# Performance work log

Measured on AMD Instinct MI355X. Metric: run time of the kernel, lower is better.

The kernel has to match this reference:

```python
import jax, jax.numpy as jnp
import numpy as np

N_NODES = 10000
W_DIM = 512
N_EDGES = 200000


def setup_inputs() -> dict:
    key = jax.random.key(0)
    k1, k2, k3 = jax.random.split(key, 3)
    z_drug = jax.random.normal(k1, (N_NODES, W_DIM), dtype=jnp.float32)
    # glorot-style init for the bilinear weight
    glorot_std = jnp.sqrt(2.0 / (W_DIM + W_DIM)).astype(jnp.float32)
    weight = jax.random.normal(k2, (W_DIM, W_DIM), dtype=jnp.float32) * glorot_std
    batch_edges = jax.random.randint(k3, (2, N_EDGES), 0, N_NODES, dtype=jnp.int64)
    return {"z_drug": z_drug, "weight": weight, "batch_edges": batch_edges}


def reference(z_drug, weight, batch_edges):
    # edge_type == 'drug_drug': both endpoints come from the drug table.
    row_embed = z_drug[batch_edges[0]]  # [E, d]
    col_embed = z_drug[batch_edges[1]]  # [E, d]
    # score_e = row_e @ W @ col_e  == diag((Z1 W) Z2^T) without the N x N blowup
    score = jnp.einsum('ed,df,ef->e', row_embed, weight, col_embed)
    return jax.nn.sigmoid(score)  # is_sigmoid=True default
```

## Files before the change

kernel.cpp:

```cpp
#include <hip/hip_runtime.h>
#include <math.h>

#define DIM     512
#define NNODES  10000
#define NEDGES  200000
#define MPAD    10048
#define NMB     157
#define NGRP    5
#define NB      (NGRP * NNODES)
#define SCAN_BLK 49
#define GEMM_GRID (NMB * 4)

using short8  = __attribute__((ext_vector_type(8))) short;
using floatx4 = __attribute__((ext_vector_type(4))) float;
using half8   = __attribute__((ext_vector_type(8))) _Float16;
using half2v  = __attribute__((ext_vector_type(2))) _Float16;

__device__ inline float dot2acc(half2v a, half2v b, float c) {
#if __has_builtin(__builtin_amdgcn_fdot2)
    return __builtin_amdgcn_fdot2(a, b, c, false);
#else
    return fmaf((float)a[0], (float)b[0], fmaf((float)a[1], (float)b[1], c));
#endif
}

#define PREP_ZBLK 2512
__global__ __launch_bounds__(256) void prep(const float* __restrict__ Z,
                                            const float* __restrict__ W,
                                            _Float16* __restrict__ Zh16,
                                            _Float16* __restrict__ Wh16t,
                                            int* __restrict__ counts) {
    const int b = blockIdx.x;
    const int t = threadIdx.x;

    if (b < 196) {
        int i = b * 256 + t;
        if (i < NB) counts[i] = 0;
    }

    if (b < PREP_ZBLK) {
        const int idx8 = (b * 256 + t) * 8;
        const int m = idx8 >> 9;
        float x[8];
        if (m < NNODES) {
            float4 v0 = *(const float4*)(Z + idx8);
            float4 v1 = *(const float4*)(Z + idx8 + 4);
            x[0]=v0.x; x[1]=v0.y; x[2]=v0.z; x[3]=v0.w;
            x[4]=v1.x; x[5]=v1.y; x[6]=v1.z; x[7]=v1.w;
        } else {
            #pragma unroll
            for (int j = 0; j < 8; ++j) x[j] = 0.f;
        }
        half8 h;
        #pragma unroll
        for (int j = 0; j < 8; ++j) h[j] = (_Float16)x[j];
        *(half8*)(Zh16 + idx8) = h;
    } else {
        __shared__ float tile[64][65];
        const int wb = b - PREP_ZBLK;
        const int kb = (wb >> 3) * 64;
        const int nb = (wb & 7) * 64;
        const int kk = t >> 2;
        const int ch = t & 3;

        const float* src = W + (size_t)(kb + kk) * DIM + nb + ch * 16;
        #pragma unroll
        for (int q = 0; q < 4; ++q) {
            float4 v = *(const float4*)(src + q * 4);
            tile[kk][ch * 16 + q * 4 + 0] = v.x;
            tile[kk][ch * 16 + q * 4 + 1] = v.y;
            tile[kk][ch * 16 + q * 4 + 2] = v.z;
            tile[kk][ch * 16 + q * 4 + 3] = v.w;
        }
        __syncthreads();

        const int nn = kk;
        half8 h0, h1;
        #pragma unroll
        for (int i = 0; i < 8; ++i) h0[i] = (_Float16)tile[ch * 16 + i][nn];
        #pragma unroll
        for (int i = 0; i < 8; ++i) h1[i] = (_Float16)tile[ch * 16 + 8 + i][nn];
        _Float16* d = Wh16t + (size_t)(nb + nn) * DIM + kb + ch * 16;
        *(half8*)(d)     = h0;
        *(half8*)(d + 8) = h1;
    }
}

__global__ __launch_bounds__(256) void gemm_f16(const _Float16* __restrict__ Zh16,
                                                const _Float16* __restrict__ Wh16t,
                                                _Float16* __restrict__ ZWh,
                                                const int* __restrict__ eidx,
                                                int* __restrict__ counts) {
    __shared__ _Float16 Abuf[2][2 * 64 * 32];
    __shared__ _Float16 Bbuf[2][2 * 128 * 32];

    const int t     = threadIdx.x;
    const int bid   = blockIdx.x;
    const int n_idx = bid & 3;
    const int m0    = (bid >> 2) * 64;
    const int n0    = n_idx * 128;

    const int l  = t & 63;
    const int w  = t >> 6;
    const int wn = w * 32;
    const int lm = l & 15;
    const int lq = l >> 4;
    const unsigned wbase = (unsigned)(t & 192);

    floatx4 acc[4][2] = {};

    auto stage = [&](int buf, int k0) {
        #pragma unroll
        for (int p = 0; p < 2; ++p) {
            const int s   = p * 256 + t;
            const int kk  = s >> 8;
            const int row = (s >> 2) & 63;
            const int ch  = s & 3;
            const _Float16* src = Zh16 + (size_t)(m0 + row) * DIM + k0 + kk * 32 + ch * 8;
            __builtin_amdgcn_global_load_lds(
                (const __attribute__((address_space(1))) void*)src,
                (__attribute__((address_space(3))) void*)&Abuf[buf][(p * 256 + wbase) * 8],
                16, 0, 0);
        }
        #pragma unroll
        for (int p = 0; p < 4; ++p) {
            const int s   = p * 256 + t;
            const int kk  = s >> 9;
            const int row = (s >> 2) & 127;
            const int ch  = s & 3;
            const _Float16* src = Wh16t + (size_t)(n0 + row) * DIM + k0 + kk * 32 + ch * 8;
            __builtin_amdgcn_global_load_lds(
                (const __attribute__((address_space(1))) void*)src,
                (__attribute__((address_space(3))) void*)&Bbuf[buf][(p * 256 + wbase) * 8],
                16, 0, 0);
        }
    };

    stage(0, 0);
    __syncthreads();

    for (int s = 0; s < 8; ++s) {
        const int buf = s & 1;
        if (s < 7) stage(buf ^ 1, (s + 1) * 64);

        #pragma unroll
        for (int kk = 0; kk < 2; ++kk) {
            half8 aF[4], bF[2];
            #pragma unroll
            for (int i = 0; i < 4; ++i)
                aF[i] = *(const half8*)&Abuf[buf][kk * 2048 + (16 * i + lm) * 32 + lq * 8];
            #pragma unroll
            for (int j = 0; j < 2; ++j)
                bF[j] = *(const half8*)&Bbuf[buf][kk * 4096 + (wn + 16 * j + lm) * 32 + lq * 8];

            #pragma unroll
            for (int i = 0; i < 4; ++i)
                #pragma unroll
                for (int j = 0; j < 2; ++j)
                    acc[i][j] = __builtin_amdgcn_mfma_f32_16x16x32_f16(aF[i], bF[j], acc[i][j], 0, 0, 0);
        }

        __syncthreads();
    }

    #pragma unroll
    for (int i = 0; i < 4; ++i)
        #pragma unroll
        for (int j = 0; j < 2; ++j)
            #pragma unroll
            for (int r = 0; r < 4; ++r) {
                const int gm = m0 + 16 * i + lq * 4 + r;
                const int gn = n0 + wn + 16 * j + lm;
                if (gm < NNODES)
                    ZWh[(size_t)gm * DIM + gn] = (_Float16)acc[i][j][r];
            }

    for (int e = bid * 256 + t; e < NEDGES; e += GEMM_GRID * 256) {
        int r = eidx[e];
        int c = eidx[NEDGES + e];
        atomicAdd(&counts[(c >> 11) * NNODES + r], 1);
    }
}

__global__ __launch_bounds__(1024) void scan_local(const int* __restrict__ counts,
                                                   int* __restrict__ partial,
                                                   int* __restrict__ blksum) {
    __shared__ int wsum[16];
    __shared__ int woff[17];
    const int t    = threadIdx.x;
    const int lane = t & 63;
    const int wv   = t >> 6;
    const int i    = blockIdx.x * 1024 + t;

    int x = (i < NB) ? counts[i] : 0;

    int v = x;
    #pragma unroll
    for (int off = 1; off < 64; off <<= 1) {
        int u = __shfl_up(v, off, 64);
        if (lane >= off) v += u;
    }
    if (lane == 63) wsum[wv] = v;
    __syncthreads();
    if (t == 0) {
        int r = 0;
        #pragma unroll
        for (int k = 0; k < 16; ++k) { woff[k] = r; r += wsum[k]; }
        woff[16] = r;
    }
    __syncthreads();

    if (i < NB) partial[i] = woff[wv] + (v - x);
    if (t == 1023) blksum[blockIdx.x] = woff[16];
}

__global__ __launch_bounds__(1024) void scan_fix(const int* __restrict__ partial,
                                                 const int* __restrict__ blksum,
                                                 int* __restrict__ cursor) {
    __shared__ int base_s;
    const int t = threadIdx.x;
    const int b = blockIdx.x;

    if (t < 64) {
        int v = (t < b) ? blksum[t] : 0;
        #pragma unroll
        for (int off = 32; off > 0; off >>= 1)
            v += __shfl_xor(v, off, 64);
        if (t == 0) base_s = v;
    }
    __syncthreads();
    const int base = base_s;

    const int i = b * 1024 + t;
    if (i < NB)
        cursor[i] = base + partial[i];
}

__global__ void scatter_edges(const int* __restrict__ eidx,
                              int* __restrict__ cursor,
                              unsigned* __restrict__ keys,
                              unsigned short* __restrict__ rows16) {
    int e = blockIdx.x * blockDim.x + threadIdx.x;
    if (e < NEDGES) {
        int r = eidx[e];
        int c = eidx[NEDGES + e];
        int pos = atomicAdd(&cursor[(c >> 11) * NNODES + r], 1);
        keys[pos]   = ((unsigned)c << 18) | (unsigned)e;
        rows16[pos] = (unsigned short)r;
    }
}

__global__ __launch_bounds__(256) void edge_score_f(const _Float16* __restrict__ ZWh,
                                                    const _Float16* __restrict__ Zh,
                                                    const unsigned* __restrict__ keys,
                                                    const unsigned short* __restrict__ rows16,
                                                    float* __restrict__ out) {
    const int t    = threadIdx.x;
    const int wgid = blockIdx.x * 4 + (t >> 6);
    const int lane = t & 63;
    const int gq   = lane >> 4;
    const int sl   = lane & 15;

    const int ii = wgid * 4 + gq;
    const unsigned k = keys[ii];
    const int c = (int)(k >> 18);
    const int r = (int)rows16[ii];

    const _Float16* rp = ZWh + (size_t)r * DIM + sl * 32;
    const _Float16* cp = Zh  + (size_t)c * DIM + sl * 32;

    half8 ra0 = *(const half8*)(rp);
    half8 ra1 = *(const half8*)(rp + 8);
    half8 ra2 = *(const half8*)(rp + 16);
    half8 ra3 = *(const half8*)(rp + 24);
    half8 c0  = *(const half8*)(cp);
    half8 c1  = *(const half8*)(cp + 8);
    half8 c2  = *(const half8*)(cp + 16);
    half8 c3  = *(const half8*)(cp + 24);

    float s = 0.f;
    #pragma unroll
    for (int d = 0; d < 4; ++d) {
        s = dot2acc((half2v){ra0[2*d], ra0[2*d+1]}, (half2v){c0[2*d], c0[2*d+1]}, s);
        s = dot2acc((half2v){ra1[2*d], ra1[2*d+1]}, (half2v){c1[2*d], c1[2*d+1]}, s);
        s = dot2acc((half2v){ra2[2*d], ra2[2*d+1]}, (half2v){c2[2*d], c2[2*d+1]}, s);
        s = dot2acc((half2v){ra3[2*d], ra3[2*d+1]}, (half2v){c3[2*d], c3[2*d+1]}, s);
    }

    s += __shfl_xor(s, 1, 64);
    s += __shfl_xor(s, 2, 64);
    s += __shfl_xor(s, 4, 64);
    s += __shfl_xor(s, 8, 64);

    if (sl == 0)
        out[k & 0x3FFFFu] = 1.0f / (1.0f + expf(-s));
}

#define GTM 128
#define GTN 64
#define GTK 16
#define LDA 132
#define LDB 68

__global__ __launch_bounds__(256) void gemm_zw(const float* __restrict__ A,
                                               const float* __restrict__ B,
                                               float* __restrict__ C) {
    __shared__ float As[GTK * LDA];
    __shared__ float Bs[GTK * LDB];

    const int t  = threadIdx.x;
    const int m0 = blockIdx.x * GTM;
    const int n0 = blockIdx.y * GTN;
    const int tx = t & 15;
    const int ty = t >> 4;

    float acc[8][4] = {};

    for (int k0 = 0; k0 < DIM; k0 += GTK) {
        #pragma unroll
        for (int p = 0; p < 2; ++p) {
            int f  = t + p * 256;
            int mm = f >> 2;
            int kq = f & 3;
            int m  = m0 + mm;
            float4 v = make_float4(0.f, 0.f, 0.f, 0.f);
            if (m < NNODES)
                v = *(const float4*)(A + (size_t)m * DIM + k0 + kq * 4);
            As[(kq * 4 + 0) * LDA + mm] = v.x;
            As[(kq * 4 + 1) * LDA + mm] = v.y;
            As[(kq * 4 + 2) * LDA + mm] = v.z;
            As[(kq * 4 + 3) * LDA + mm] = v.w;
        }
        {
            int kb = t >> 4, n4 = t & 15;
            *(float4*)&Bs[kb * LDB + n4 * 4] =
                *(const float4*)(B + (size_t)(k0 + kb) * DIM + n0 + n4 * 4);
        }
        __syncthreads();

        #pragma unroll
        for (int kk = 0; kk < GTK; ++kk) {
            float4 a0 = *(const float4*)&As[kk * LDA + ty * 8];
            float4 a1 = *(const float4*)&As[kk * LDA + ty * 8 + 4];
            float4 b  = *(const float4*)&Bs[kk * LDB + tx * 4];
            float av[8] = {a0.x, a0.y, a0.z, a0.w, a1.x, a1.y, a1.z, a1.w};
            float bv[4] = {b.x, b.y, b.z, b.w};
            #pragma unroll
            for (int i = 0; i < 8; ++i)
                #pragma unroll
                for (int j = 0; j < 4; ++j)
                    acc[i][j] = fmaf(av[i], bv[j], acc[i][j]);
        }
        __syncthreads();
    }

    #pragma unroll
    for (int i = 0; i < 8; ++i) {
        int m = m0 + ty * 8 + i;
        if (m < NNODES)
            *(float4*)(C + (size_t)m * DIM + n0 + tx * 4) =
                make_float4(acc[i][0], acc[i][1], acc[i][2], acc[i][3]);
    }
}

__global__ __launch_bounds__(256) void edge_score(const float* __restrict__ ZW,
                                                  const float* __restrict__ Z,
                                                  const int* __restrict__ eidx,
                                                  float* __restrict__ out) {
    const int e    = blockIdx.x * 4 + (threadIdx.x >> 6);
    const int lane = threadIdx.x & 63;

    const int r = eidx[e];
    const int c = eidx[NEDGES + e];

    const float4* pr = (const float4*)(ZW + (size_t)r * DIM);
    const float4* pc = (const float4*)(Z  + (size_t)c * DIM);

    float4 a0 = pr[lane * 2 + 0];
    float4 a1 = pr[lane * 2 + 1];
    float4 b0 = pc[lane * 2 + 0];
    float4 b1 = pc[lane * 2 + 1];

    float s = a0.x * b0.x;
    s = fmaf(a0.y, b0.y, s);
    s = fmaf(a0.z, b0.z, s);
    s = fmaf(a0.w, b0.w, s);
    s = fmaf(a1.x, b1.x, s);
    s = fmaf(a1.y, b1.y, s);
    s = fmaf(a1.z, b1.z, s);
    s = fmaf(a1.w, b1.w, s);

    #pragma unroll
    for (int off = 32; off > 0; off >>= 1)
        s += __shfl_xor(s, off, 64);

    if (lane == 0)
        out[e] = 1.0f / (1.0f + expf(-s));
}

extern "C" void kernel_launch(void* const* d_in, const int* in_sizes, int n_in,
                              void* d_out, int out_size, void* d_ws, size_t ws_size,
                              hipStream_t stream) {
    const float* Z  = (const float*)d_in[0];
    const float* W  = (const float*)d_in[1];
    const int*   EI = (const int*)d_in[2];
    float* out = (float*)d_out;

    char* p = (char*)d_ws;
    _Float16* ZWh   = (_Float16*)p;  p += (size_t)MPAD * DIM * 2;
    _Float16* Zh16  = (_Float16*)p;  p += (size_t)MPAD * DIM * 2;
    _Float16* Wh16t = (_Float16*)p;  p += (size_t)DIM * DIM * 2;
    int* counts  = (int*)p;          p += (size_t)NB * 4;
    int* cursor  = (int*)p;          p += (size_t)NB * 4;
    int* partial = (int*)p;          p += (size_t)NB * 4;
    int* blksum  = (int*)p;          p += (size_t)SCAN_BLK * 4;
    unsigned* keys = (unsigned*)p;   p += (size_t)NEDGES * 4;
    unsigned short* rows16 = (unsigned short*)p; p += (size_t)NEDGES * 2;
    const size_t need_full = (size_t)(p - (char*)d_ws);

    if (ws_size >= need_full) {
        prep<<<PREP_ZBLK + 64, 256, 0, stream>>>(Z, W, Zh16, Wh16t, counts);
        gemm_f16<<<GEMM_GRID, 256, 0, stream>>>(Zh16, Wh16t, ZWh, EI, counts);
        scan_local<<<SCAN_BLK, 1024, 0, stream>>>(counts, partial, blksum);
        scan_fix<<<SCAN_BLK, 1024, 0, stream>>>(partial, blksum, cursor);
        scatter_edges<<<(NEDGES + 255) / 256, 256, 0, stream>>>(EI, cursor, keys, rows16);
        edge_score_f<<<NEDGES / 16, 256, 0, stream>>>(ZWh, Zh16, keys, rows16, out);
    } else {
        float* ZW = (float*)d_ws;
        dim3 g1((NNODES + GTM - 1) / GTM, DIM / GTN);
        gemm_zw<<<g1, 256, 0, stream>>>(Z, W, ZW);
        edge_score<<<NEDGES / 4, 256, 0, stream>>>(ZW, Z, EI, out);
    }
}
```

Measured before the change: 136.1 us.

## Fuse histogram, scan and scatter into GEMM launch with flag-based inter-block sync

Merges the separate GEMM, two scan kernels and scatter kernel into one persistent-style launch. Dedicated block ranges do the histogram, a decoupled scan using global atomic flags, and the edge scatter, running concurrently with the GEMM blocks. The aim is to remove three kernel launches and their serialization gaps and to overlap the sort with the GEMM. The risk is a deadlock if the waiting blocks are resident while the blocks they depend on cannot be scheduled, although the low block indices are likely dispatched first.

```diff
diff --git a/kernel.cpp b/kernel.cpp
--- a/kernel.cpp
+++ b/kernel.cpp
@@ -8,10 +8,16 @@
 #define NMB     157
 #define NGRP    5
 #define NB      (NGRP * NNODES)
-#define SCAN_BLK 49
+#define SCAN_N  49
 #define GEMM_GRID (NMB * 4)
 
-using short8  = __attribute__((ext_vector_type(8))) short;
+#define HIST_BLK   50
+#define SCAN_BASE  50
+#define SCAT_BASE  99
+#define SCAT_N     98
+#define GEMM_BASE  197
+#define FUSE_GRID  (GEMM_BASE + GEMM_GRID)
+
 using floatx4 = __attribute__((ext_vector_type(4))) float;
 using half8   = __attribute__((ext_vector_type(8))) _Float16;
 using half2v  = __attribute__((ext_vector_type(2))) _Float16;
@@ -24,14 +30,31 @@
 #endif
 }
 
+__device__ inline int aload(const int* p) {
+    return __hip_atomic_load(p, __ATOMIC_RELAXED, __HIP_MEMORY_SCOPE_AGENT);
+}
+__device__ inline void astore(int* p, int v) {
+    __hip_atomic_store(p, v, __ATOMIC_RELAXED, __HIP_MEMORY_SCOPE_AGENT);
+}
+__device__ inline void waitflag(int* f, int target) {
+    while (__hip_atomic_load(f, __ATOMIC_ACQUIRE, __HIP_MEMORY_SCOPE_AGENT) < target)
+        __builtin_amdgcn_s_sleep(4);
+}
+__device__ inline void signal(int* f) {
+    __hip_atomic_fetch_add(f, 1, __ATOMIC_RELEASE, __HIP_MEMORY_SCOPE_AGENT);
+}
+
 #define PREP_ZBLK 2512
 __global__ __launch_bounds__(256) void prep(const float* __restrict__ Z,
                                             const float* __restrict__ W,
                                             _Float16* __restrict__ Zh16,
                                             _Float16* __restrict__ Wh16t,
-                                            int* __restrict__ counts) {
+                                            int* __restrict__ counts,
+                                            int* __restrict__ flags) {
     const int b = blockIdx.x;
     const int t = threadIdx.x;
+
+    if (b == 0 && t < 4) flags[t] = 0;
 
     if (b < 196) {
         int i = b * 256 + t;
@@ -86,167 +109,197 @@
     }
 }
 
-__global__ __launch_bounds__(256) void gemm_f16(const _Float16* __restrict__ Zh16,
-                                                const _Float16* __restrict__ Wh16t,
-                                                _Float16* __restrict__ ZWh,
-                                                const int* __restrict__ eidx,
-                                                int* __restrict__ counts) {
+__global__ __launch_bounds__(256, 3) void gemm_sort(
+        const _Float16* __restrict__ Zh16,
+        const _Float16* __restrict__ Wh16t,
+        _Float16* __restrict__ ZWh,
+        const int* __restrict__ eidx,
+        int* __restrict__ counts,
+        int* __restrict__ cursor,
+        int* __restrict__ blksum,
+        unsigned* __restrict__ keys,
+        unsigned short* __restrict__ rows16,
+        int* __restrict__ flags)
+{
     __shared__ _Float16 Abuf[2][2 * 64 * 32];
     __shared__ _Float16 Bbuf[2][2 * 128 * 32];
-
-    const int t     = threadIdx.x;
-    const int bid   = blockIdx.x;
-    const int n_idx = bid & 3;
-    const int m0    = (bid >> 2) * 64;
-    const int n0    = n_idx * 128;
-
-    const int l  = t & 63;
-    const int w  = t >> 6;
-    const int wn = w * 32;
-    const int lm = l & 15;
-    const int lq = l >> 4;
-    const unsigned wbase = (unsigned)(t & 192);
-
-    floatx4 acc[4][2] = {};
-
-    auto stage = [&](int buf, int k0) {
-        #pragma unroll
-        for (int p = 0; p < 2; ++p) {
-            const int s   = p * 256 + t;
-            const int kk  = s >> 8;
-            const int row = (s >> 2) & 63;
-            const int ch  = s & 3;
-            const _Float16* src = Zh16 + (size_t)(m0 + row) * DIM + k0 + kk * 32 + ch * 8;
-            __builtin_amdgcn_global_load_lds(
-                (const __attribute__((address_space(1))) void*)src,
-                (__attribute__((address_space(3))) void*)&Abuf[buf][(p * 256 + wbase) * 8],
-                16, 0, 0);
-        }
-        #pragma unroll
-        for (int p = 0; p < 4; ++p) {
-            const int s   = p * 256 + t;
-            const int kk  = s >> 9;
-            const int row = (s >> 2) & 127;
-            const int ch  = s & 3;
-            const _Float16* src = Wh16t + (size_t)(n0 + row) * DIM + k0 + kk * 32 + ch * 8;
-            __builtin_amdgcn_global_load_lds(
-                (const __attribute__((address_space(1))) void*)src,
-                (__attribute__((address_space(3))) void*)&Bbuf[buf][(p * 256 + wbase) * 8],
-                16, 0, 0);
-        }
-    };
-
-    stage(0, 0);
-    __syncthreads();
-
-    for (int s = 0; s < 8; ++s) {
-        const int buf = s & 1;
-        if (s < 7) stage(buf ^ 1, (s + 1) * 64);
-
-        #pragma unroll
-        for (int kk = 0; kk < 2; ++kk) {
-            half8 aF[4], bF[2];
-            #pragma unroll
-            for (int i = 0; i < 4; ++i)
-                aF[i] = *(const half8*)&Abuf[buf][kk * 2048 + (16 * i + lm) * 32 + lq * 8];
-            #pragma unroll
-            for (int j = 0; j < 2; ++j)
-                bF[j] = *(const half8*)&Bbuf[buf][kk * 4096 + (wn + 16 * j + lm) * 32 + lq * 8];
-
-            #pragma unroll
-            for (int i = 0; i < 4; ++i)
+    __shared__ int wsum[4];
+    __shared__ int sbase;
+
+    const int t   = threadIdx.x;
+    const int bid = blockIdx.x;
+
+    if (bid >= GEMM_BASE) {
+        const int vb    = bid - GEMM_BASE;
+        const int n_idx = vb & 3;
+        const int m0    = (vb >> 2) * 64;
+        const int n0    = n_idx * 128;
+
+        const int l  = t & 63;
+        const int w  = t >> 6;
+        const int wn = w * 32;
+        const int lm = l & 15;
+        const int lq = l >> 4;
+        const unsigned wbase = (unsigned)(t & 192);
+
+        floatx4 acc[4][2] = {};
+
+        auto stage = [&](int buf, int k0) {
+            #pragma unroll
+            for (int p = 0; p < 2; ++p) {
+                const int s   = p * 256 + t;
+                const int kk  = s >> 8;
+                const int row = (s >> 2) & 63;
+                const int ch  = s & 3;
+                const _Float16* src = Zh16 + (size_t)(m0 + row) * DIM + k0 + kk * 32 + ch * 8;
+                __builtin_amdgcn_global_load_lds(
+                    (const __attribute__((address_space(1))) void*)src,
+                    (__attribute__((address_space(3))) void*)&Abuf[buf][(p * 256 + wbase) * 8],
+                    16, 0, 0);
+            }
+            #pragma unroll
+            for (int p = 0; p < 4; ++p) {
+                const int s   = p * 256 + t;
+                const int kk  = s >> 9;
+                const int row = (s >> 2) & 127;
+                const int ch  = s & 3;
+                const _Float16* src = Wh16t + (size_t)(n0 + row) * DIM + k0 + kk * 32 + ch * 8;
+                __builtin_amdgcn_global_load_lds(
+                    (const __attribute__((address_space(1))) void*)src,
+                    (__attribute__((address_space(3))) void*)&Bbuf[buf][(p * 256 + wbase) * 8],
+                    16, 0, 0);
+            }
+        };
+
+        stage(0, 0);
+        __syncthreads();
+
+        for (int s = 0; s < 8; ++s) {
+            const int buf = s & 1;
+            if (s < 7) stage(buf ^ 1, (s + 1) * 64);
+
+            #pragma unroll
+            for (int kk = 0; kk < 2; ++kk) {
+                half8 aF[4], bF[2];
+                #pragma unroll
+                for (int i = 0; i < 4; ++i)
+                    aF[i] = *(const half8*)&Abuf[buf][kk * 2048 + (16 * i + lm) * 32 + lq * 8];
                 #pragma unroll
                 for (int j = 0; j < 2; ++j)
-                    acc[i][j] = __builtin_amdgcn_mfma_f32_16x16x32_f16(aF[i], bF[j], acc[i][j], 0, 0, 0);
-        }
-
-        __syncthreads();
-    }
-
-    #pragma unroll
-    for (int i = 0; i < 4; ++i)
-        #pragma unroll
-        for (int j = 0; j < 2; ++j)
-            #pragma unroll
-            for (int r = 0; r < 4; ++r) {
-                const int gm = m0 + 16 * i + lq * 4 + r;
-                const int gn = n0 + wn + 16 * j + lm;
-                if (gm < NNODES)
-                    ZWh[(size_t)gm * DIM + gn] = (_Float16)acc[i][j][r];
+                    bF[j] = *(const half8*)&Bbuf[buf][kk * 4096 + (wn + 16 * j + lm) * 32 + lq * 8];
+
+                #pragma unroll
+                for (int i = 0; i < 4; ++i)
+                    #pragma unroll
+                    for (int j = 0; j < 2; ++j)
+                        acc[i][j] = __builtin_amdgcn_mfma_f32_16x16x32_f16(aF[i], bF[j], acc[i][j], 0, 0, 0);
             }
-
-    for (int e = bid * 256 + t; e < NEDGES; e += GEMM_GRID * 256) {
-        int r = eidx[e];
-        int c = eidx[NEDGES + e];
-        atomicAdd(&counts[(c >> 11) * NNODES + r], 1);
-    }
-}
-
-__global__ __launch_bounds__(1024) void scan_local(const int* __restrict__ counts,
-                                                   int* __restrict__ partial,
-                                                   int* __restrict__ blksum) {
-    __shared__ int wsum[16];
-    __shared__ int woff[17];
-    const int t    = threadIdx.x;
-    const int lane = t & 63;
-    const int wv   = t >> 6;
-    const int i    = blockIdx.x * 1024 + t;
-
-    int x = (i < NB) ? counts[i] : 0;
-
-    int v = x;
-    #pragma unroll
-    for (int off = 1; off < 64; off <<= 1) {
-        int u = __shfl_up(v, off, 64);
-        if (lane >= off) v += u;
-    }
-    if (lane == 63) wsum[wv] = v;
-    __syncthreads();
-    if (t == 0) {
-        int r = 0;
-        #pragma unroll
-        for (int k = 0; k < 16; ++k) { woff[k] = r; r += wsum[k]; }
-        woff[16] = r;
-    }
-    __syncthreads();
-
-    if (i < NB) partial[i] = woff[wv] + (v - x);
-    if (t == 1023) blksum[blockIdx.x] = woff[16];
-}
-
-__global__ __launch_bounds__(1024) void scan_fix(const int* __restrict__ partial,
-                                                 const int* __restrict__ blksum,
-                                                 int* __restrict__ cursor) {
-    __shared__ int base_s;
-    const int t = threadIdx.x;
-    const int b = blockIdx.x;
-
-    if (t < 64) {
-        int v = (t < b) ? blksum[t] : 0;
-        #pragma unroll
-        for (int off = 32; off > 0; off >>= 1)
-            v += __shfl_xor(v, off, 64);
-        if (t == 0) base_s = v;
-    }
-    __syncthreads();
-    const int base = base_s;
-
-    const int i = b * 1024 + t;
-    if (i < NB)
-        cursor[i] = base + partial[i];
-}
-
-__global__ void scatter_edges(const int* __restrict__ eidx,
-                              int* __restrict__ cursor,
-                              unsigned* __restrict__ keys,
-                              unsigned short* __restrict__ rows16) {
-    int e = blockIdx.x * blockDim.x + threadIdx.x;
-    if (e < NEDGES) {
-        int r = eidx[e];
-        int c = eidx[NEDGES + e];
-        int pos = atomicAdd(&cursor[(c >> 11) * NNODES + r], 1);
-        keys[pos]   = ((unsigned)c << 18) | (unsigned)e;
-        rows16[pos] = (unsigned short)r;
+            __syncthreads();
+        }
+
+        #pragma unroll
+        for (int i = 0; i < 4; ++i)
+            #pragma unroll
+            for (int j = 0; j < 2; ++j)
+                #pragma unroll
+                for (int r = 0; r < 4; ++r) {
+                    const int gm = m0 + 16 * i + lq * 4 + r;
+                    const int gn = n0 + wn + 16 * j + lm;
+                    if (gm < NNODES)
+                        ZWh[(size_t)gm * DIM + gn] = (_Float16)acc[i][j][r];
+                }
+        return;
+    }
+
+    if (bid < HIST_BLK) {
+        for (int e = bid * 256 + t; e < NEDGES; e += HIST_BLK * 256) {
+            int r = eidx[e];
+            int c = eidx[NEDGES + e];
+            atomicAdd(&counts[(c >> 11) * NNODES + r], 1);
+        }
+        __syncthreads();
+        if (t == 0) signal(&flags[0]);
+        return;
+    }
+
+    if (bid < SCAT_BASE) {
+        const int b = bid - SCAN_BASE;
+        const int lane = t & 63;
+        const int wv   = t >> 6;
+
+        if (t == 0) waitflag(&flags[0], HIST_BLK);
+        __syncthreads();
+
+        const int base = b * 1024 + t * 4;
+        int v0 = 0, v1 = 0, v2 = 0, v3 = 0;
+        if (base + 3 < NB) {
+            v0 = aload(counts + base);
+            v1 = aload(counts + base + 1);
+            v2 = aload(counts + base + 2);
+            v3 = aload(counts + base + 3);
+        } else {
+            if (base     < NB) v0 = aload(counts + base);
+            if (base + 1 < NB) v1 = aload(counts + base + 1);
+            if (base + 2 < NB) v2 = aload(counts + base + 2);
+        }
+        const int ts = v0 + v1 + v2 + v3;
+        int incl = ts;
+        #pragma unroll
+        for (int off = 1; off < 64; off <<= 1) {
+            int u = __shfl_up(incl, off, 64);
+            if (lane >= off) incl += u;
+        }
+        if (lane == 63) wsum[wv] = incl;
+        __syncthreads();
+        int wb = 0;
+        #pragma unroll
+        for (int k = 0; k < 4; ++k) if (k < wv) wb += wsum[k];
+        const int ex   = wb + incl - ts;
+        const int pre0 = ex;
+        const int pre1 = ex + v0;
+        const int pre2 = pre1 + v1;
+        const int pre3 = pre2 + v2;
+        if (t == 255) astore(blksum + b, wb + incl);
+        __syncthreads();
+        if (t == 0) { signal(&flags[1]); waitflag(&flags[1], SCAN_N); }
+        __syncthreads();
+
+        if (t < 64) {
+            int v = (t < b) ? aload(blksum + t) : 0;
+            #pragma unroll
+            for (int off = 32; off > 0; off >>= 1)
+                v += __shfl_xor(v, off, 64);
+            if (t == 0) sbase = v;
+        }
+        __syncthreads();
+        const int b0 = sbase;
+
+        if (base + 3 < NB) {
+            astore(cursor + base,     b0 + pre0);
+            astore(cursor + base + 1, b0 + pre1);
+            astore(cursor + base + 2, b0 + pre2);
+            astore(cursor + base + 3, b0 + pre3);
+        } else {
+            if (base     < NB) astore(cursor + base,     b0 + pre0);
+            if (base + 1 < NB) astore(cursor + base + 1, b0 + pre1);
+            if (base + 2 < NB) astore(cursor + base + 2, b0 + pre2);
+        }
+        __syncthreads();
+        if (t == 0) signal(&flags[2]);
+        return;
+    }
+
+    {
+        if (t == 0) waitflag(&flags[2], SCAN_N);
+        __syncthreads();
+
+        for (int e = (bid - SCAT_BASE) * 256 + t; e < NEDGES; e += SCAT_N * 256) {
+            int r = eidx[e];
+            int c = eidx[NEDGES + e];
+            int pos = atomicAdd(&cursor[(c >> 11) * NNODES + r], 1);
+            keys[pos]   = ((unsigned)c << 18) | (unsigned)e;
+            rows16[pos] = (unsigned short)r;
+        }
     }
 }
 
@@ -412,18 +465,16 @@
     _Float16* Wh16t = (_Float16*)p;  p += (size_t)DIM * DIM * 2;
     int* counts  = (int*)p;          p += (size_t)NB * 4;
     int* cursor  = (int*)p;          p += (size_t)NB * 4;
-    int* partial = (int*)p;          p += (size_t)NB * 4;
-    int* blksum  = (int*)p;          p += (size_t)SCAN_BLK * 4;
+    int* blksum  = (int*)p;          p += (size_t)SCAN_N * 4;
     unsigned* keys = (unsigned*)p;   p += (size_t)NEDGES * 4;
     unsigned short* rows16 = (unsigned short*)p; p += (size_t)NEDGES * 2;
+    int* flags = (int*)p;            p += 4 * 4;
     const size_t need_full = (size_t)(p - (char*)d_ws);
 
     if (ws_size >= need_full) {
-        prep<<<PREP_ZBLK + 64, 256, 0, stream>>>(Z, W, Zh16, Wh16t, counts);
-        gemm_f16<<<GEMM_GRID, 256, 0, stream>>>(Zh16, Wh16t, ZWh, EI, counts);
-        scan_local<<<SCAN_BLK, 1024, 0, stream>>>(counts, partial, blksum);
-        scan_fix<<<SCAN_BLK, 1024, 0, stream>>>(partial, blksum, cursor);
-        scatter_edges<<<(NEDGES + 255) / 256, 256, 0, stream>>>(EI, cursor, keys, rows16);
+        prep<<<PREP_ZBLK + 64, 256, 0, stream>>>(Z, W, Zh16, Wh16t, counts, flags);
+        gemm_sort<<<FUSE_GRID, 256, 0, stream>>>(Zh16, Wh16t, ZWh, EI, counts,
+                                                 cursor, blksum, keys, rows16, flags);
         edge_score_f<<<NEDGES / 16, 256, 0, stream>>>(ZWh, Zh16, keys, rows16, out);
     } else {
         float* ZW = (float*)d_ws;
```

Measured after the change: 184.8 us. 1.36x slower.
